# Kernel tuning notes

Hardware: AMD Instinct MI355X
Metric: run time of the kernel (lower is better)

Reference implementation:

```python
import jax, jax.numpy as jnp
import numpy as np
import math

B, S, D, H, HD, W, G = 2, 4096, 768, 12, 64, 256, 64  # batch, seq, embed, heads, head_dim, one-sided window, n global tokens


def _chunk_keys(k, w):
    # k: [B,S,H,HD] -> overlapping 3w-wide key windows per w-sized query chunk: [B,nc,3w,H,HD]
    Bz, S_, Hh, HDd = k.shape
    nc = S_ // w
    kp = jnp.pad(k, ((0, 0), (w, w), (0, 0), (0, 0)))
    kb = kp.reshape(Bz, nc + 2, w, Hh, HDd)
    return jnp.concatenate([kb[:, 0:nc], kb[:, 1:nc + 1], kb[:, 2:nc + 2]], axis=2)


def _band_qk(q, k, w):
    # banded scores: out[b,i,h,j] = q_i . k_{i+j-w}, j in [0, 2w]
    Bz, S_, Hh, HDd = q.shape
    nc = S_ // w
    qc = q.reshape(Bz, nc, w, Hh, HDd)
    kc = _chunk_keys(k, w)
    sc = jnp.einsum('bcphd,bckhd->bchpk', qc, kc)  # [B,nc,H,w,3w]
    rows = jnp.arange(w)[:, None]
    cols = rows + jnp.arange(2 * w + 1)[None, :]   # within-window key index = p + j
    band = sc[:, :, :, rows, cols]                 # [B,nc,H,w,2w+1]
    return band.transpose(0, 1, 3, 2, 4).reshape(Bz, S_, Hh, 2 * w + 1)


def _band_pv(p, v, w):
    # out[b,i,h,:] = sum_j p[b,i,h,j] * v[b, i+j-w, h, :]
    Bz, S_, Hh, K = p.shape
    HDd = v.shape[-1]
    nc = S_ // w
    pc = p.reshape(Bz, nc, w, Hh, K).transpose(0, 1, 3, 2, 4)  # [B,nc,H,w,2w+1]
    rows = jnp.arange(w)[:, None]
    cols = rows + jnp.arange(2 * w + 1)[None, :]
    full = jnp.zeros((Bz, nc, Hh, w, 3 * w), p.dtype).at[:, :, :, rows, cols].set(pc)
    vc = _chunk_keys(v, w)
    out = jnp.einsum('bchpk,bckhd->bcphd', full, vc)  # [B,nc,w,H,HD]
    return out.reshape(Bz, S_, Hh, HDd)


def setup_inputs() -> dict:
    key = jax.random.key(0)
    ks = jax.random.split(key, 4)
    std = 0.02
    # attention mask: +1 = global (first G tokens), 0 = local windowed, no padding
    attention_mask = jnp.concatenate(
        [jnp.ones((B, G), jnp.int32), jnp.zeros((B, S - G), jnp.int32)], axis=1)
    return {
        'hidden_states': jax.random.normal(ks[0], (B, S, D), jnp.float32),
        'attention_mask': attention_mask,
        'Wq': jax.random.normal(ks[1], (D, D), jnp.float32) * std,
        'bq': jnp.zeros((D,), jnp.float32),
        'Wk': jax.random.normal(ks[2], (D, D), jnp.float32) * std,
        'bk': jnp.zeros((D,), jnp.float32),
        'Wv': jax.random.normal(ks[3], (D, D), jnp.float32) * std,
        'bv': jnp.zeros((D,), jnp.float32),
    }


def reference(hidden_states, attention_mask, Wq, bq, Wk, bk, Wv, bv):
    Bz, S_, D_ = hidden_states.shape
    HDd = D_ // H
    q = ((hidden_states @ Wq.T + bq) / math.sqrt(HDd)).reshape(Bz, S_, H, HDd)
    k = (hidden_states @ Wk.T + bk).reshape(Bz, S_, H, HDd)
    v = (hidden_states @ Wv.T + bv).reshape(Bz, S_, H, HDd)

    band = _band_qk(q, k, W)  # [B,S,H,2W+1]

    i = jnp.arange(S_)
    key_abs = i[:, None] + jnp.arange(2 * W + 1)[None, :] - W  # [S,2W+1]
    valid = (key_abs >= 0) & (key_abs < S_)
    kac = jnp.clip(key_abs, 0, S_ - 1)
    is_glob = attention_mask != 0                       # [B,S]
    glob_at_key = is_glob[:, kac] & valid[None]          # [B,S,2W+1]
    # remove global keys from windowed attention: d_mask = -10000 * head_dim (ones @ float_mask)
    band = band + jnp.where(glob_at_key, jnp.float32(-10000.0 * HDd), jnp.float32(0.0))[:, :, None, :]
    # mask_invalid_locations: out-of-range diagonals -> -inf
    band = jnp.where(valid[None, :, None, :], band, -jnp.inf)

    # global-token attention (first G tokens are the global ones)
    gs = jnp.einsum('bihd,bghd->bihg', q, k[:, :G])      # [B,S,H,G]

    scores = jnp.concatenate([gs, band], axis=-1)        # [B,S,H,G+2W+1]
    probs = jax.nn.softmax(scores.astype(jnp.float32), axis=-1)

    attn = jnp.einsum('bihg,bghd->bihd', probs[..., :G], v[:, :G]) + _band_pv(probs[..., G:], v, W)
    # [B,S,H,HD] -> (seq_len, bsz, embed_dim) as in the torch module
    return jnp.transpose(attn, (1, 0, 2, 3)).reshape(S_, Bz, D_)
```

## Files before the change

### kernel.cpp

```cpp
#include <hip/hip_runtime.h>
#include <hip/hip_bf16.h>
#include <stdint.h>

typedef __attribute__((ext_vector_type(4))) float          f32x4;
typedef __attribute__((ext_vector_type(4))) float          f4;
typedef __attribute__((ext_vector_type(2))) unsigned int   u32x2;
typedef __bf16 bf16_t;
typedef __attribute__((ext_vector_type(8))) bf16_t         bf16x8;
typedef __attribute__((ext_vector_type(8))) unsigned short u16x8;

#define NB 2
#define NS 4096
#define ND 768
#define NH 12
#define NW 256

__device__ __forceinline__ unsigned short f2bf(float f) {
  union { float f; unsigned u; } v; v.f = f;
  unsigned r = v.u + 0x7fffu + ((v.u >> 16) & 1u);
  return (unsigned short)(r >> 16);
}

__device__ __forceinline__ void gload16(const void* g, void* l) {
  __builtin_amdgcn_global_load_lds((const __attribute__((address_space(1))) void*)g,
                                   (__attribute__((address_space(3))) void*)l, 16, 0, 0);
}

__global__ void cast_kernel(const float* __restrict__ in, unsigned short* __restrict__ out, int n4) {
  int i = blockIdx.x * blockDim.x + threadIdx.x;
  int stride = gridDim.x * blockDim.x;
  for (; i < n4; i += stride) {
    f4 v = reinterpret_cast<const f4*>(in)[i];
    unsigned u0 = (unsigned)f2bf(v.x) | ((unsigned)f2bf(v.y) << 16);
    unsigned u1 = (unsigned)f2bf(v.z) | ((unsigned)f2bf(v.w) << 16);
    u32x2 o = {u0, u1};
    reinterpret_cast<u32x2*>(out)[i] = o;
  }
}

__global__ __launch_bounds__(256) void qkv_gemm(
    const unsigned short* __restrict__ Ab,
    const unsigned short* __restrict__ Wqb,
    const unsigned short* __restrict__ Wkb,
    const unsigned short* __restrict__ Wvb,
    const float* __restrict__ bqp, const float* __restrict__ bkp, const float* __restrict__ bvp,
    unsigned short* __restrict__ Qw, unsigned short* __restrict__ Kw, unsigned short* __restrict__ Vw) {
  __shared__ unsigned short As[128 * 32];
  __shared__ unsigned short Bs[128 * 32];

  int bid = blockIdx.x;
  int bn = bid % 18, bm = bid / 18;
  int mat = bn / 6, bnn = bn % 6;
  const unsigned short* Wm = (mat == 0) ? Wqb : ((mat == 1) ? Wkb : Wvb);
  const float* bias = (mat == 0) ? bqp : ((mat == 1) ? bkp : bvp);
  unsigned short* dst = (mat == 0) ? Qw : ((mat == 1) ? Kw : Vw);

  int t = threadIdx.x;
  int w = t >> 6, l = t & 63;
  int lg = l >> 4, ln = l & 15;
  int wm = w & 1, wn = w >> 1;

  f32x4 acc[4][4];
#pragma unroll
  for (int i = 0; i < 4; i++)
#pragma unroll
    for (int j = 0; j < 4; j++) acc[i][j] = f32x4{0.f, 0.f, 0.f, 0.f};

  for (int kt = 0; kt < 24; ++kt) {
    __syncthreads();
#pragma unroll
    for (int is = 0; is < 2; ++is) {
      int chunk = is * 256 + t;
      int row = chunk >> 2;
      int c8 = (chunk & 3) * 8;
      gload16(Ab + ((size_t)(bm * 128 + row)) * 768 + kt * 32 + c8, As + chunk * 8);
      gload16(Wm + ((size_t)(bnn * 128 + row)) * 768 + kt * 32 + c8, Bs + chunk * 8);
    }
    __syncthreads();
    bf16x8 af[4], bfr[4];
#pragma unroll
    for (int i = 0; i < 4; i++) {
      af[i]  = *reinterpret_cast<const bf16x8*>(As + (wm * 64 + i * 16 + ln) * 32 + lg * 8);
      bfr[i] = *reinterpret_cast<const bf16x8*>(Bs + (wn * 64 + i * 16 + ln) * 32 + lg * 8);
    }
#pragma unroll
    for (int i = 0; i < 4; i++)
#pragma unroll
      for (int j = 0; j < 4; j++)
        acc[i][j] = __builtin_amdgcn_mfma_f32_16x16x32_bf16(af[i], bfr[j], acc[i][j], 0, 0, 0);
  }

#pragma unroll
  for (int j = 0; j < 4; j++) {
    int col = bnn * 128 + wn * 64 + j * 16 + ln;
    float bv_ = bias[col];
    int hh = col >> 6, dd = col & 63;
#pragma unroll
    for (int i = 0; i < 4; i++) {
#pragma unroll
      for (int r = 0; r < 4; r++) {
        int tok = bm * 128 + wm * 64 + i * 16 + lg * 4 + r;
        int bb = tok >> 12, ss = tok & 4095;
        float v = acc[i][j][r] + bv_;
        if (mat == 0) v *= 0.125f;
        dst[(((size_t)bb * 12 + hh) * 4096 + ss) * 64 + dd] = f2bf(v);
      }
    }
  }
}

__global__ __launch_bounds__(256) void attn_kernel(
    const unsigned short* __restrict__ Qw,
    const unsigned short* __restrict__ Kw,
    const unsigned short* __restrict__ Vw,
    const int* __restrict__ amask,
    float* __restrict__ out) {
  __shared__ unsigned short Ks[64 * 64];
  __shared__ unsigned short Vt[64 * 64];
  __shared__ unsigned short Ps[4][16 * 72];

  int bid = blockIdx.x;
  int qc = bid & 63;
  int bh = bid >> 6;
  int b = bh / 12;
  int hh = bh % 12;
  int qbase = qc * 64;

  int t = threadIdx.x, w = t >> 6, l = t & 63;
  int lg = l >> 4, ln = l & 15;

  const unsigned short* Qbh = Qw + (size_t)bh * (NS * 64);
  const unsigned short* Kbh = Kw + (size_t)bh * (NS * 64);
  const unsigned short* Vbh = Vw + (size_t)bh * (NS * 64);
  const int* mrow = amask + b * NS;

  bf16x8 qf[2];
  {
    const unsigned short* qp = Qbh + (size_t)(qbase + w * 16 + ln) * 64 + lg * 8;
    qf[0] = *reinterpret_cast<const bf16x8*>(qp);
    qf[1] = *reinterpret_cast<const bf16x8*>(qp + 32);
  }

  float m_r[4] = {-1e30f, -1e30f, -1e30f, -1e30f};
  float l_r[4] = {0.f, 0.f, 0.f, 0.f};
  f32x4 oacc[4];
#pragma unroll
  for (int i = 0; i < 4; i++) oacc[i] = f32x4{0.f, 0.f, 0.f, 0.f};

  int q0 = qbase + w * 16 + lg * 4;

  for (int tt = -1; tt < 9; ++tt) {
    int key0 = (tt < 0) ? 0 : (qbase - 256 + tt * 64);
    if (key0 < 0 || key0 >= NS) continue;

    __syncthreads();
#pragma unroll
    for (int is = 0; is < 2; ++is) {
      int chunk = is * 256 + t;
      int krow = chunk >> 3, gran = chunk & 7;
      gload16(Kbh + (size_t)(key0 + krow) * 64 + (gran ^ (krow & 7)) * 8, Ks + chunk * 8);
    }
    u16x8 vv[2];
#pragma unroll
    for (int is = 0; is < 2; ++is) {
      int g = is * 256 + t;
      int key = g & 63, d0 = (g >> 6) * 8;
      vv[is] = *reinterpret_cast<const u16x8*>(Vbh + (size_t)(key0 + key) * 64 + d0);
    }
#pragma unroll
    for (int is = 0; is < 2; ++is) {
      int g = is * 256 + t;
      int key = g & 63, d0 = (g >> 6) * 8;
#pragma unroll
      for (int j = 0; j < 8; ++j) {
        int d = d0 + j;
        Vt[d * 64 + (key ^ ((d & 7) << 3))] = vv[is][j];
      }
    }
    __syncthreads();

    f32x4 sa[4];
#pragma unroll
    for (int nt = 0; nt < 4; nt++) sa[nt] = f32x4{0.f, 0.f, 0.f, 0.f};
#pragma unroll
    for (int nt = 0; nt < 4; nt++) {
      int key = nt * 16 + ln;
#pragma unroll
      for (int ks = 0; ks < 2; ++ks) {
        int dby = (ks * 64 + lg * 16) ^ ((key & 7) << 4);
        bf16x8 kf = *reinterpret_cast<const bf16x8*>(Ks + key * 64 + (dby >> 1));
        sa[nt] = __builtin_amdgcn_mfma_f32_16x16x32_bf16(qf[ks], kf, sa[nt], 0, 0, 0);
      }
    }

    if (tt >= 0) {
#pragma unroll
      for (int nt = 0; nt < 4; nt++) {
        int ka = key0 + nt * 16 + ln;
        int sup = mrow[ka];
#pragma unroll
        for (int r = 0; r < 4; r++) {
          int qa = q0 + r;
          bool ok = (sup == 0) && (ka >= qa - NW) && (ka <= qa + NW);
          if (!ok) sa[nt][r] = -1e30f;
        }
      }
    }

    float scl[4];
#pragma unroll
    for (int r = 0; r < 4; r++) {
      float v = fmaxf(fmaxf(sa[0][r], sa[1][r]), fmaxf(sa[2][r], sa[3][r]));
      v = fmaxf(v, __shfl_xor(v, 1, 64));
      v = fmaxf(v, __shfl_xor(v, 2, 64));
      v = fmaxf(v, __shfl_xor(v, 4, 64));
      v = fmaxf(v, __shfl_xor(v, 8, 64));
      float mn = fmaxf(m_r[r], v);
      scl[r] = __expf(m_r[r] - mn);
      m_r[r] = mn;
    }
#pragma unroll
    for (int r = 0; r < 4; r++) {
      float s = 0.f;
#pragma unroll
      for (int nt = 0; nt < 4; nt++) {
        float p = __expf(sa[nt][r] - m_r[r]);
        sa[nt][r] = p;
        s += p;
      }
      s += __shfl_xor(s, 1, 64);
      s += __shfl_xor(s, 2, 64);
      s += __shfl_xor(s, 4, 64);
      s += __shfl_xor(s, 8, 64);
      l_r[r] = l_r[r] * scl[r] + s;
    }
#pragma unroll
    for (int nt = 0; nt < 4; nt++)
#pragma unroll
      for (int r = 0; r < 4; r++) oacc[nt][r] *= scl[r];

    unsigned short* pw = &Ps[w][0];
#pragma unroll
    for (int nt = 0; nt < 4; nt++)
#pragma unroll
      for (int r = 0; r < 4; r++)
        pw[(lg * 4 + r) * 72 + nt * 16 + ln] = f2bf(sa[nt][r]);

#pragma unroll
    for (int ks = 0; ks < 2; ++ks) {
      bf16x8 pf = *reinterpret_cast<const bf16x8*>(pw + ln * 72 + ks * 32 + lg * 8);
#pragma unroll
      for (int nt = 0; nt < 4; ++nt) {
        int d = nt * 16 + ln;
        int eoff = (ks * 32 + lg * 8) ^ ((d & 7) << 3);
        bf16x8 vf = *reinterpret_cast<const bf16x8*>(Vt + d * 64 + eoff);
        oacc[nt] = __builtin_amdgcn_mfma_f32_16x16x32_bf16(pf, vf, oacc[nt], 0, 0, 0);
      }
    }
  }

#pragma unroll
  for (int nt = 0; nt < 4; nt++) {
    int d = nt * 16 + ln;
#pragma unroll
    for (int r = 0; r < 4; r++) {
      int qa = q0 + r;
      out[((size_t)qa * NB + b) * ND + hh * 64 + d] = oacc[nt][r] / l_r[r];
    }
  }
}

extern "C" void kernel_launch(void* const* d_in, const int* in_sizes, int n_in,
                              void* d_out, int out_size, void* d_ws, size_t ws_size,
                              hipStream_t stream) {
  (void)in_sizes; (void)n_in; (void)out_size; (void)ws_size;
  const float* hidden = (const float*)d_in[0];
  const int*   amask  = (const int*)d_in[1];
  const float* Wq = (const float*)d_in[2];
  const float* bq = (const float*)d_in[3];
  const float* Wk = (const float*)d_in[4];
  const float* bk = (const float*)d_in[5];
  const float* Wv = (const float*)d_in[6];
  const float* bv = (const float*)d_in[7];
  float* out = (float*)d_out;

  char* p = (char*)d_ws;
  unsigned short* hb  = (unsigned short*)p; p += (size_t)8192 * 768 * 2;
  unsigned short* wqb = (unsigned short*)p; p += (size_t)768 * 768 * 2;
  unsigned short* wkb = (unsigned short*)p; p += (size_t)768 * 768 * 2;
  unsigned short* wvb = (unsigned short*)p; p += (size_t)768 * 768 * 2;
  unsigned short* Qws = (unsigned short*)p; p += (size_t)24 * 4096 * 64 * 2;
  unsigned short* Kws = (unsigned short*)p; p += (size_t)24 * 4096 * 64 * 2;
  unsigned short* Vws = (unsigned short*)p; p += (size_t)24 * 4096 * 64 * 2;

  cast_kernel<<<1024, 256, 0, stream>>>(hidden, hb, 8192 * 768 / 4);
  cast_kernel<<<576, 256, 0, stream>>>(Wq, wqb, 768 * 768 / 4);
  cast_kernel<<<576, 256, 0, stream>>>(Wk, wkb, 768 * 768 / 4);
  cast_kernel<<<576, 256, 0, stream>>>(Wv, wvb, 768 * 768 / 4);
  qkv_gemm<<<64 * 18, 256, 0, stream>>>(hb, wqb, wkb, wvb, bq, bk, bv, Qws, Kws, Vws);
  attn_kernel<<<24 * 64, 256, 0, stream>>>(Qws, Kws, Vws, amask, out);
}
```

Before: 206.8 us.

## Enlarge attention query tile to 128, remap blocks per XCD, fuse weight casts

The attention kernel now runs 512 threads per block, so each block covers 128 queries and each K/V tile loaded into shared memory serves twice as many queries. The V transpose store is rewritten to pack two keys into one 32-bit write, which halves the shared-memory store count. Block indices in both the GEMM and attention kernels are remapped so that contiguous logical tiles land on the same XCD, which should improve L2 locality. The three weight-cast launches are merged into one kernel to cut launch overhead. The larger blocks halve the grid and may lower occupancy, and the 128-query tile walks one extra 64-key tile at its edges.

```diff
diff --git a/kernel.cpp b/kernel.cpp
--- a/kernel.cpp
+++ b/kernel.cpp
@@ -8,6 +8,7 @@
 typedef __bf16 bf16_t;
 typedef __attribute__((ext_vector_type(8))) bf16_t         bf16x8;
 typedef __attribute__((ext_vector_type(8))) unsigned short u16x8;
+typedef __attribute__((ext_vector_type(4))) unsigned short u16x4;
 
 #define NB 2
 #define NS 4096
@@ -38,6 +39,24 @@
   }
 }
 
+__global__ void cast3_kernel(const float* __restrict__ w0, const float* __restrict__ w1,
+                             const float* __restrict__ w2, unsigned short* __restrict__ o0,
+                             unsigned short* __restrict__ o1, unsigned short* __restrict__ o2) {
+  const int n4 = 768 * 768 / 4;
+  int i = blockIdx.x * blockDim.x + threadIdx.x;
+  int stride = gridDim.x * blockDim.x;
+  for (; i < 3 * n4; i += stride) {
+    int m = i / n4, j = i - m * n4;
+    const float* in = (m == 0) ? w0 : ((m == 1) ? w1 : w2);
+    unsigned short* out = (m == 0) ? o0 : ((m == 1) ? o1 : o2);
+    f4 v = reinterpret_cast<const f4*>(in)[j];
+    unsigned u0 = (unsigned)f2bf(v.x) | ((unsigned)f2bf(v.y) << 16);
+    unsigned u1 = (unsigned)f2bf(v.z) | ((unsigned)f2bf(v.w) << 16);
+    u32x2 o = {u0, u1};
+    reinterpret_cast<u32x2*>(out)[j] = o;
+  }
+}
+
 __global__ __launch_bounds__(256) void qkv_gemm(
     const unsigned short* __restrict__ Ab,
     const unsigned short* __restrict__ Wqb,
@@ -48,8 +67,9 @@
   __shared__ unsigned short As[128 * 32];
   __shared__ unsigned short Bs[128 * 32];
 
-  int bid = blockIdx.x;
-  int bn = bid % 18, bm = bid / 18;
+  int phys = blockIdx.x;
+  int logical = (phys & 7) * 144 + (phys >> 3);
+  int bn = logical % 18, bm = logical / 18;
   int mat = bn / 6, bnn = bn % 6;
   const unsigned short* Wm = (mat == 0) ? Wqb : ((mat == 1) ? Wkb : Wvb);
   const float* bias = (mat == 0) ? bqp : ((mat == 1) ? bkp : bvp);
@@ -109,7 +129,7 @@
   }
 }
 
-__global__ __launch_bounds__(256) void attn_kernel(
+__global__ __launch_bounds__(512) void attn_kernel(
     const unsigned short* __restrict__ Qw,
     const unsigned short* __restrict__ Kw,
     const unsigned short* __restrict__ Vw,
@@ -117,14 +137,15 @@
     float* __restrict__ out) {
   __shared__ unsigned short Ks[64 * 64];
   __shared__ unsigned short Vt[64 * 64];
-  __shared__ unsigned short Ps[4][16 * 72];
-
-  int bid = blockIdx.x;
-  int qc = bid & 63;
-  int bh = bid >> 6;
+  __shared__ unsigned short Ps[8][16 * 72];
+
+  int phys = blockIdx.x;
+  int logical = (phys & 7) * 96 + (phys >> 3);
+  int qc = logical & 31;
+  int bh = logical >> 5;
   int b = bh / 12;
   int hh = bh % 12;
-  int qbase = qc * 64;
+  int qbase = qc * 128;
 
   int t = threadIdx.x, w = t >> 6, l = t & 63;
   int lg = l >> 4, ln = l & 15;
@@ -149,32 +170,26 @@
 
   int q0 = qbase + w * 16 + lg * 4;
 
-  for (int tt = -1; tt < 9; ++tt) {
+  for (int tt = -1; tt < 10; ++tt) {
     int key0 = (tt < 0) ? 0 : (qbase - 256 + tt * 64);
     if (key0 < 0 || key0 >= NS) continue;
 
     __syncthreads();
-#pragma unroll
-    for (int is = 0; is < 2; ++is) {
-      int chunk = is * 256 + t;
-      int krow = chunk >> 3, gran = chunk & 7;
-      gload16(Kbh + (size_t)(key0 + krow) * 64 + (gran ^ (krow & 7)) * 8, Ks + chunk * 8);
-    }
-    u16x8 vv[2];
-#pragma unroll
-    for (int is = 0; is < 2; ++is) {
-      int g = is * 256 + t;
-      int key = g & 63, d0 = (g >> 6) * 8;
-      vv[is] = *reinterpret_cast<const u16x8*>(Vbh + (size_t)(key0 + key) * 64 + d0);
-    }
-#pragma unroll
-    for (int is = 0; is < 2; ++is) {
-      int g = is * 256 + t;
-      int key = g & 63, d0 = (g >> 6) * 8;
-#pragma unroll
-      for (int j = 0; j < 8; ++j) {
+    {
+      int krow = t >> 3, gran = t & 7;
+      gload16(Kbh + (size_t)(key0 + krow) * 64 + (gran ^ (krow & 7)) * 8, Ks + t * 8);
+    }
+    {
+      int p2 = t & 31;
+      int d0 = (t >> 5) * 4;
+      const unsigned short* vp0 = Vbh + (size_t)(key0 + 2 * p2) * 64 + d0;
+      u16x4 va = *reinterpret_cast<const u16x4*>(vp0);
+      u16x4 vb = *reinterpret_cast<const u16x4*>(vp0 + 64);
+#pragma unroll
+      for (int j = 0; j < 4; ++j) {
         int d = d0 + j;
-        Vt[d * 64 + (key ^ ((d & 7) << 3))] = vv[is][j];
+        unsigned val = (unsigned)va[j] | ((unsigned)vb[j] << 16);
+        *reinterpret_cast<unsigned*>(Vt + d * 64 + ((2 * p2) ^ ((d & 7) << 3))) = val;
       }
     }
     __syncthreads();
@@ -294,9 +309,7 @@
   unsigned short* Vws = (unsigned short*)p; p += (size_t)24 * 4096 * 64 * 2;
 
   cast_kernel<<<1024, 256, 0, stream>>>(hidden, hb, 8192 * 768 / 4);
-  cast_kernel<<<576, 256, 0, stream>>>(Wq, wqb, 768 * 768 / 4);
-  cast_kernel<<<576, 256, 0, stream>>>(Wk, wkb, 768 * 768 / 4);
-  cast_kernel<<<576, 256, 0, stream>>>(Wv, wvb, 768 * 768 / 4);
+  cast3_kernel<<<432, 256, 0, stream>>>(Wq, Wk, Wv, wqb, wkb, wvb);
   qkv_gemm<<<64 * 18, 256, 0, stream>>>(hb, wqb, wkb, wvb, bq, bk, bv, Qws, Kws, Vws);
-  attn_kernel<<<24 * 64, 256, 0, stream>>>(Qws, Kws, Vws, amask, out);
-}
+  attn_kernel<<<24 * 32, 512, 0, stream>>>(Qws, Kws, Vws, amask, out);
+}
```

New measurement: 212.5 us. 2.8% more time.
